# Kernel optimization log

Hardware: AMD Instinct MI355X
Metric: run time of the kernel (lower is better)

The kernel has to match this reference:

```python
import jax, jax.numpy as jnp
import numpy as np

DIST_THR = 0.2
CONTACT_TGT = 0.1
ALPHA = 0.01
HUBER_DELTA = 0.01
W_BCE = 0.5
W_DIST = 1.0
EPS = 1e-06


def setup_inputs() -> dict:
    key = jax.random.key(0)
    k1, k2, k3, k4 = jax.random.split(key, 4)
    BT, Vh, Vo = 16, 6890, 2048
    return {
        "human_verts": jax.random.uniform(k1, (BT, Vh, 3), dtype=jnp.float32),
        "object_verts": jax.random.uniform(k2, (BT, Vo, 3), dtype=jnp.float32),
        "gt_human_verts": jax.random.uniform(k3, (BT, Vh, 3), dtype=jnp.float32),
        "gt_object_verts": jax.random.uniform(k4, (BT, Vo, 3), dtype=jnp.float32),
    }


def _min_cdist(A, B):
    # A:[BT,NA,3], B:[BT,NB,3] -> min Euclidean distance over B: [BT,NA]
    aa = jnp.sum(A * A, axis=-1)               # [BT,NA]
    bb = jnp.sum(B * B, axis=-1)               # [BT,NB]
    ab = jnp.einsum("bnd,bmd->bnm", A, B)      # [BT,NA,NB]
    d2 = aa[:, :, None] + bb[:, None, :] - 2.0 * ab
    d = jnp.sqrt(jnp.maximum(d2, 0.0))
    return jnp.min(d, axis=-1)


def _bce_balanced(p, target):
    p = jnp.clip(p, 1e-06, 1.0 - 1e-06)
    pos = jnp.sum(target)
    neg = target.size - pos
    pos_w = (neg + EPS) / (pos + EPS)
    w = jnp.where(target > 0.5, pos_w, 1.0)
    loss = -(target * jnp.log(p) + (1.0 - target) * jnp.log(1.0 - p))
    return jnp.mean(w * loss)


def _masked_huber(over, mask):
    m = (mask > 0.5).astype(over.dtype)
    ax = jnp.abs(over)
    hub = jnp.where(ax < HUBER_DELTA, 0.5 * ax * ax / HUBER_DELTA, ax - 0.5 * HUBER_DELTA)
    cnt = jnp.sum(m)
    s = jnp.sum(hub * m)
    return jnp.where(cnt > 0, s / jnp.maximum(cnt, 1.0), 0.0)


def reference(human_verts, object_verts, gt_human_verts, gt_object_verts):
    dmin_h = _min_cdist(human_verts, object_verts)      # [BT,Vh]
    dmin_o = _min_cdist(object_verts, human_verts)      # [BT,Vo]
    dmin_h_gt = _min_cdist(gt_human_verts, gt_object_verts)
    dmin_o_gt = _min_cdist(gt_object_verts, gt_human_verts)
    gt_mask_h = (dmin_h_gt < DIST_THR).astype(jnp.float32)
    gt_mask_o = (dmin_o_gt < DIST_THR).astype(jnp.float32)

    inv_alpha = 1.0 / max(ALPHA, 1e-08)
    p_h = jax.nn.sigmoid((DIST_THR - dmin_h) * inv_alpha)
    p_o = jax.nn.sigmoid((DIST_THR - dmin_o) * inv_alpha)
    L_bce = 0.5 * (_bce_balanced(p_h, gt_mask_h) + _bce_balanced(p_o, gt_mask_o))

    over_h = jnp.maximum(dmin_h - CONTACT_TGT, 0.0)
    over_o = jnp.maximum(dmin_o - CONTACT_TGT, 0.0)
    L_dist = _masked_huber(over_h, gt_mask_h) + _masked_huber(over_o, gt_mask_o)

    return W_BCE * L_bce + W_DIST * L_dist
```

## Files before the change

### kernel.cpp

```cpp
#include <hip/hip_runtime.h>
#include <math.h>


#define BT 16
#define VH 6890
#define VO 2048
#define NH (BT * VH)
#define NO (BT * VO)

typedef float v2f __attribute__((ext_vector_type(2)));

#define RP 4

__global__ __launch_bounds__(256, 4)
void mindist_all(const float* __restrict__ hv,  const float* __restrict__ ov,
                 const float* __restrict__ ghv, const float* __restrict__ gov,
                 unsigned int* __restrict__ dh,  unsigned int* __restrict__ dov,
                 unsigned int* __restrict__ dhg, unsigned int* __restrict__ dog)
{
    __shared__ float4 lds[256];

    const int idx = blockIdx.x;
    const float *A, *B;
    unsigned int* out;
    int nA, nB, bt, abk, sliceLen, b0;

    if (idx < 1024) {
        const int p = idx >> 9;
        const int r = idx & 511;
        abk = r & 3;
        bt  = (r >> 2) & 15;
        const int z = r >> 6;
        A = p ? ghv : hv;  B = p ? gov : ov;  out = p ? dhg : dh;
        nA = VH; nB = VO; sliceLen = 256; b0 = z * 256;
    } else {
        const int q = idx - 1024;
        const int p = q >> 9;
        const int r = q & 511;
        abk = 0;
        bt  = r & 15;
        const int z = r >> 4;
        A = p ? gov : ov;  B = p ? ghv : hv;  out = p ? dog : dov;
        nA = VO; nB = VH; sliceLen = 216; b0 = z * 216;
    }

    const float* Ab = A + (size_t)bt * nA * 3;
    const float* Bb = B + (size_t)bt * nB * 3;
    const int tid = threadIdx.x;

    if (tid < sliceLen) {
        const int gj = b0 + tid;
        float4 w;
        if (gj < nB) {
            const float bx = Bb[gj * 3 + 0];
            const float by = Bb[gj * 3 + 1];
            const float bz = Bb[gj * 3 + 2];
            w = make_float4(-2.f * bx, -2.f * by, -2.f * bz,
                            fmaf(bx, bx, fmaf(by, by, bz * bz)));
        } else {
            w = make_float4(0.f, 0.f, 0.f, 3.0e38f);
        }
        lds[tid] = w;
    }

    const int rowb = abk * 2048 + tid;
    v2f ax[RP], ay[RP], az[RP], rmin[RP];
#pragma unroll
    for (int k = 0; k < RP; ++k) {
        const int r0 = rowb + (2 * k    ) * 256;
        const int r1 = rowb + (2 * k + 1) * 256;
        const int i0 = (r0 < nA) ? r0 : 0;
        const int i1 = (r1 < nA) ? r1 : 0;
        ax[k] = (v2f){Ab[i0 * 3 + 0], Ab[i1 * 3 + 0]};
        ay[k] = (v2f){Ab[i0 * 3 + 1], Ab[i1 * 3 + 1]};
        az[k] = (v2f){Ab[i0 * 3 + 2], Ab[i1 * 3 + 2]};
        rmin[k] = (v2f){3.0e38f, 3.0e38f};
    }

    __syncthreads();

    for (int j = 0; j < sliceLen; j += 4) {
#pragma unroll
        for (int u = 0; u < 4; ++u) {
            const float4 b = lds[j + u];
            const v2f nbx = (v2f){b.x, b.x};
            const v2f nby = (v2f){b.y, b.y};
            const v2f nbz = (v2f){b.z, b.z};
            const v2f bbv = (v2f){b.w, b.w};
#pragma unroll
            for (int k = 0; k < RP; ++k) {
                v2f t = __builtin_elementwise_fma(az[k], nbz, bbv);
                t     = __builtin_elementwise_fma(ay[k], nby, t);
                t     = __builtin_elementwise_fma(ax[k], nbx, t);
                rmin[k] = __builtin_elementwise_min(rmin[k], t);
            }
        }
    }

#pragma unroll
    for (int k = 0; k < RP; ++k) {
        const int r0 = rowb + (2 * k    ) * 256;
        const int r1 = rowb + (2 * k + 1) * 256;
        if (r0 < nA) {
            const float aa = fmaf(ax[k].x, ax[k].x, fmaf(ay[k].x, ay[k].x, az[k].x * az[k].x));
            const float v  = fmaxf(aa + rmin[k].x, 0.f);
            atomicMin(&out[(size_t)bt * nA + r0], __float_as_uint(v));
        }
        if (r1 < nA) {
            const float aa = fmaf(ax[k].y, ax[k].y, fmaf(ay[k].y, ay[k].y, az[k].y * az[k].y));
            const float v  = fmaxf(aa + rmin[k].y, 0.f);
            atomicMin(&out[(size_t)bt * nA + r1], __float_as_uint(v));
        }
    }
}

#define NBLK_H 431
#define NBLK_O 128

__global__ __launch_bounds__(256)
void reduce_loss_all(const float* __restrict__ dh2, const float* __restrict__ dhg2,
                     const float* __restrict__ do2, const float* __restrict__ dog2,
                     float* __restrict__ acc)
{
    const int b = blockIdx.x;
    const float *p2, *g2;
    float* a4;
    int N, i0;
    if (b < NBLK_H) { p2 = dh2; g2 = dhg2; a4 = acc;     N = NH; i0 = b * 256; }
    else            { p2 = do2; g2 = dog2; a4 = acc + 4; N = NO; i0 = (b - NBLK_H) * 256; }

    const int i = i0 + threadIdx.x;
    float t = 0.f, sp = 0.f, sn = 0.f, sh = 0.f;
    if (i < N) {
        const float d  = sqrtf(p2[i]);
        const float dg = sqrtf(g2[i]);
        const float tt = (dg < 0.2f) ? 1.f : 0.f;

        const float z = (0.2f - d) * 100.0f;
        float p = 1.0f / (1.0f + expf(-z));
        p = fminf(fmaxf(p, 1e-6f), 1.0f - 1e-6f);
        const float bce = (tt > 0.5f) ? -logf(p) : -logf(1.0f - p);

        const float over = fmaxf(d - 0.1f, 0.0f);
        const float hub  = (over < 0.01f) ? (0.5f * over * over) / 0.01f
                                          : (over - 0.5f * 0.01f);
        t  = tt;
        sp = tt * bce;
        sn = (1.0f - tt) * bce;
        sh = tt * hub;
    }
    for (int off = 32; off > 0; off >>= 1) {
        t  += __shfl_down(t,  off);
        sp += __shfl_down(sp, off);
        sn += __shfl_down(sn, off);
        sh += __shfl_down(sh, off);
    }
    __shared__ float wsum[4][4];
    const int wid = threadIdx.x >> 6, lane = threadIdx.x & 63;
    if (lane == 0) {
        wsum[wid][0] = t; wsum[wid][1] = sp; wsum[wid][2] = sn; wsum[wid][3] = sh;
    }
    __syncthreads();
    if (threadIdx.x == 0) {
        float s0 = 0, s1 = 0, s2 = 0, s3 = 0;
        for (int w = 0; w < 4; ++w) {
            s0 += wsum[w][0]; s1 += wsum[w][1]; s2 += wsum[w][2]; s3 += wsum[w][3];
        }
        atomicAdd(&a4[0], s0);
        atomicAdd(&a4[1], s1);
        atomicAdd(&a4[2], s2);
        atomicAdd(&a4[3], s3);
    }
}

__global__ void finalize_kernel(const float* __restrict__ acc, float* __restrict__ out)
{
    const float Ph = acc[0], SpH = acc[1], SnH = acc[2], ShH = acc[3];
    const float Po = acc[4], SpO = acc[5], SnO = acc[6], ShO = acc[7];
    const float Nh = (float)NH;
    const float No = (float)NO;

    const float pwH = ((Nh - Ph) + 1e-6f) / (Ph + 1e-6f);
    const float pwO = ((No - Po) + 1e-6f) / (Po + 1e-6f);
    const float bceH = (pwH * SpH + SnH) / Nh;
    const float bceO = (pwO * SpO + SnO) / No;
    const float Lbce = 0.5f * (bceH + bceO);

    const float LdH = (Ph > 0.f) ? ShH / fmaxf(Ph, 1.f) : 0.f;
    const float LdO = (Po > 0.f) ? ShO / fmaxf(Po, 1.f) : 0.f;
    const float Ldist = LdH + LdO;

    out[0] = 0.5f * Lbce + 1.0f * Ldist;
}

extern "C" void kernel_launch(void* const* d_in, const int* in_sizes, int n_in,
                              void* d_out, int out_size, void* d_ws, size_t ws_size,
                              hipStream_t stream)
{
    const float* hv  = (const float*)d_in[0];
    const float* ov  = (const float*)d_in[1];
    const float* ghv = (const float*)d_in[2];
    const float* gov = (const float*)d_in[3];

    float* ws  = (float*)d_ws;
    float* dh  = ws;
    float* dov = dh  + NH;
    float* dhg = dov + NO;
    float* dog = dhg + NH;
    float* acc = dog + NO;

    hipMemsetAsync(ws, 0x7f, (size_t)(2 * (NH + NO)) * sizeof(float), stream);
    hipMemsetAsync(acc, 0, 8 * sizeof(float), stream);

    mindist_all<<<2048, 256, 0, stream>>>(hv, ov, ghv, gov,
                                          (unsigned int*)dh, (unsigned int*)dov,
                                          (unsigned int*)dhg, (unsigned int*)dog);

    reduce_loss_all<<<NBLK_H + NBLK_O, 256, 0, stream>>>(dh, dhg, dov, dog, acc);

    finalize_kernel<<<1, 1, 0, stream>>>(acc, (float*)d_out);
}
```

Measured before the change: 163.6 us.

## Use inline packed FMA with op_sel broadcasts and min3, fuse finalize into reduce

The inner distance loop now uses inline-asm v_pk_fma_f32 with op_sel to broadcast B coordinates straight from packed LDS pairs, removing the per-element broadcast moves. It also merges two candidate minima with v_min3_f32. Launch bounds rise to 8 waves per SIMD to raise occupancy. The accumulator memset and the finalize kernel are replaced by zeroing inside the first kernel and a last-block-done pattern in the reduce kernel, which drops one memset and one launch. Risks are register pressure under the tighter launch bound and correctness of the hand-written op_sel encodings.

```diff
diff --git a/kernel.cpp b/kernel.cpp
--- a/kernel.cpp
+++ b/kernel.cpp
@@ -12,13 +12,28 @@
 
 #define RP 4
 
-__global__ __launch_bounds__(256, 4)
+#define PK_FMA_ZB(t, a, q) \
+    asm("v_pk_fma_f32 %0, %1, %2, %2 op_sel:[0,0,1] op_sel_hi:[1,0,1]" \
+        : "=v"(t) : "v"(a), "v"(q))
+#define PK_FMA_YB(t, a, p) \
+    asm("v_pk_fma_f32 %0, %1, %2, %0 op_sel:[0,1,0] op_sel_hi:[1,1,1]" \
+        : "+v"(t) : "v"(a), "v"(p))
+#define PK_FMA_XB(t, a, p) \
+    asm("v_pk_fma_f32 %0, %1, %2, %0 op_sel:[0,0,0] op_sel_hi:[1,0,1]" \
+        : "+v"(t) : "v"(a), "v"(p))
+#define MIN3(r, x, y) \
+    asm("v_min3_f32 %0, %1, %2, %0" : "+v"(r) : "v"(x), "v"(y))
+
+__global__ __launch_bounds__(256, 8)
 void mindist_all(const float* __restrict__ hv,  const float* __restrict__ ov,
                  const float* __restrict__ ghv, const float* __restrict__ gov,
                  unsigned int* __restrict__ dh,  unsigned int* __restrict__ dov,
-                 unsigned int* __restrict__ dhg, unsigned int* __restrict__ dog)
+                 unsigned int* __restrict__ dhg, unsigned int* __restrict__ dog,
+                 unsigned int* __restrict__ accw)
 {
-    __shared__ float4 lds[256];
+    __shared__ v2f lds2[512];
+
+    if (blockIdx.x == 0 && threadIdx.x < 12) accw[threadIdx.x] = 0u;
 
     const int idx = blockIdx.x;
     const float *A, *B;
@@ -50,21 +65,21 @@
 
     if (tid < sliceLen) {
         const int gj = b0 + tid;
-        float4 w;
         if (gj < nB) {
             const float bx = Bb[gj * 3 + 0];
             const float by = Bb[gj * 3 + 1];
             const float bz = Bb[gj * 3 + 2];
-            w = make_float4(-2.f * bx, -2.f * by, -2.f * bz,
-                            fmaf(bx, bx, fmaf(by, by, bz * bz)));
+            lds2[2 * tid + 0] = (v2f){-2.f * bx, -2.f * by};
+            lds2[2 * tid + 1] = (v2f){-2.f * bz, fmaf(bx, bx, fmaf(by, by, bz * bz))};
         } else {
-            w = make_float4(0.f, 0.f, 0.f, 3.0e38f);
-        }
-        lds[tid] = w;
+            lds2[2 * tid + 0] = (v2f){0.f, 0.f};
+            lds2[2 * tid + 1] = (v2f){0.f, 3.0e38f};
+        }
     }
 
     const int rowb = abk * 2048 + tid;
-    v2f ax[RP], ay[RP], az[RP], rmin[RP];
+    v2f ax[RP], ay[RP], az[RP];
+    float rx[RP], ry[RP];
 #pragma unroll
     for (int k = 0; k < RP; ++k) {
         const int r0 = rowb + (2 * k    ) * 256;
@@ -74,25 +89,30 @@
         ax[k] = (v2f){Ab[i0 * 3 + 0], Ab[i1 * 3 + 0]};
         ay[k] = (v2f){Ab[i0 * 3 + 1], Ab[i1 * 3 + 1]};
         az[k] = (v2f){Ab[i0 * 3 + 2], Ab[i1 * 3 + 2]};
-        rmin[k] = (v2f){3.0e38f, 3.0e38f};
+        rx[k] = 3.0e38f; ry[k] = 3.0e38f;
     }
 
     __syncthreads();
 
-    for (int j = 0; j < sliceLen; j += 4) {
-#pragma unroll
-        for (int u = 0; u < 4; ++u) {
-            const float4 b = lds[j + u];
-            const v2f nbx = (v2f){b.x, b.x};
-            const v2f nby = (v2f){b.y, b.y};
-            const v2f nbz = (v2f){b.z, b.z};
-            const v2f bbv = (v2f){b.w, b.w};
+    for (int j0 = 0; j0 < sliceLen; j0 += 8) {
+        const v2f* base = &lds2[2 * j0];
+#pragma unroll
+        for (int jj = 0; jj < 4; ++jj) {
+            const v2f p0 = base[4 * jj + 0];
+            const v2f q0 = base[4 * jj + 1];
+            const v2f p1 = base[4 * jj + 2];
+            const v2f q1 = base[4 * jj + 3];
 #pragma unroll
             for (int k = 0; k < RP; ++k) {
-                v2f t = __builtin_elementwise_fma(az[k], nbz, bbv);
-                t     = __builtin_elementwise_fma(ay[k], nby, t);
-                t     = __builtin_elementwise_fma(ax[k], nbx, t);
-                rmin[k] = __builtin_elementwise_min(rmin[k], t);
+                v2f tA, tB;
+                PK_FMA_ZB(tA, az[k], q0);
+                PK_FMA_YB(tA, ay[k], p0);
+                PK_FMA_XB(tA, ax[k], p0);
+                PK_FMA_ZB(tB, az[k], q1);
+                PK_FMA_YB(tB, ay[k], p1);
+                PK_FMA_XB(tB, ax[k], p1);
+                MIN3(rx[k], tA.x, tB.x);
+                MIN3(ry[k], tA.y, tB.y);
             }
         }
     }
@@ -103,24 +123,23 @@
         const int r1 = rowb + (2 * k + 1) * 256;
         if (r0 < nA) {
             const float aa = fmaf(ax[k].x, ax[k].x, fmaf(ay[k].x, ay[k].x, az[k].x * az[k].x));
-            const float v  = fmaxf(aa + rmin[k].x, 0.f);
-            atomicMin(&out[(size_t)bt * nA + r0], __float_as_uint(v));
+            atomicMin(&out[(size_t)bt * nA + r0], __float_as_uint(fmaxf(aa + rx[k], 0.f)));
         }
         if (r1 < nA) {
             const float aa = fmaf(ax[k].y, ax[k].y, fmaf(ay[k].y, ay[k].y, az[k].y * az[k].y));
-            const float v  = fmaxf(aa + rmin[k].y, 0.f);
-            atomicMin(&out[(size_t)bt * nA + r1], __float_as_uint(v));
+            atomicMin(&out[(size_t)bt * nA + r1], __float_as_uint(fmaxf(aa + ry[k], 0.f)));
         }
     }
 }
 
 #define NBLK_H 431
 #define NBLK_O 128
+#define NBLK   (NBLK_H + NBLK_O)
 
 __global__ __launch_bounds__(256)
-void reduce_loss_all(const float* __restrict__ dh2, const float* __restrict__ dhg2,
+void reduce_finalize(const float* __restrict__ dh2, const float* __restrict__ dhg2,
                      const float* __restrict__ do2, const float* __restrict__ dog2,
-                     float* __restrict__ acc)
+                     float* __restrict__ acc, float* __restrict__ outp)
 {
     const int b = blockIdx.x;
     const float *p2, *g2;
@@ -170,27 +189,28 @@
         atomicAdd(&a4[1], s1);
         atomicAdd(&a4[2], s2);
         atomicAdd(&a4[3], s3);
-    }
-}
-
-__global__ void finalize_kernel(const float* __restrict__ acc, float* __restrict__ out)
-{
-    const float Ph = acc[0], SpH = acc[1], SnH = acc[2], ShH = acc[3];
-    const float Po = acc[4], SpO = acc[5], SnO = acc[6], ShO = acc[7];
-    const float Nh = (float)NH;
-    const float No = (float)NO;
-
-    const float pwH = ((Nh - Ph) + 1e-6f) / (Ph + 1e-6f);
-    const float pwO = ((No - Po) + 1e-6f) / (Po + 1e-6f);
-    const float bceH = (pwH * SpH + SnH) / Nh;
-    const float bceO = (pwO * SpO + SnO) / No;
-    const float Lbce = 0.5f * (bceH + bceO);
-
-    const float LdH = (Ph > 0.f) ? ShH / fmaxf(Ph, 1.f) : 0.f;
-    const float LdO = (Po > 0.f) ? ShO / fmaxf(Po, 1.f) : 0.f;
-    const float Ldist = LdH + LdO;
-
-    out[0] = 0.5f * Lbce + 1.0f * Ldist;
+
+        __threadfence();
+        const unsigned f = atomicAdd((unsigned int*)&acc[8], 1u);
+        if (f == NBLK - 1) {
+            float v[8];
+            for (int q = 0; q < 8; ++q) v[q] = atomicAdd(&acc[q], 0.0f);
+            const float Ph = v[0], SpH = v[1], SnH = v[2], ShH = v[3];
+            const float Po = v[4], SpO = v[5], SnO = v[6], ShO = v[7];
+            const float Nh = (float)NH, No = (float)NO;
+
+            const float pwH = ((Nh - Ph) + 1e-6f) / (Ph + 1e-6f);
+            const float pwO = ((No - Po) + 1e-6f) / (Po + 1e-6f);
+            const float bceH = (pwH * SpH + SnH) / Nh;
+            const float bceO = (pwO * SpO + SnO) / No;
+            const float Lbce = 0.5f * (bceH + bceO);
+
+            const float LdH = (Ph > 0.f) ? ShH / fmaxf(Ph, 1.f) : 0.f;
+            const float LdO = (Po > 0.f) ? ShO / fmaxf(Po, 1.f) : 0.f;
+
+            outp[0] = 0.5f * Lbce + (LdH + LdO);
+        }
+    }
 }
 
 extern "C" void kernel_launch(void* const* d_in, const int* in_sizes, int n_in,
@@ -210,13 +230,11 @@
     float* acc = dog + NO;
 
     hipMemsetAsync(ws, 0x7f, (size_t)(2 * (NH + NO)) * sizeof(float), stream);
-    hipMemsetAsync(acc, 0, 8 * sizeof(float), stream);
 
     mindist_all<<<2048, 256, 0, stream>>>(hv, ov, ghv, gov,
                                           (unsigned int*)dh, (unsigned int*)dov,
-                                          (unsigned int*)dhg, (unsigned int*)dog);
-
-    reduce_loss_all<<<NBLK_H + NBLK_O, 256, 0, stream>>>(dh, dhg, dov, dog, acc);
-
-    finalize_kernel<<<1, 1, 0, stream>>>(acc, (float*)d_out);
+                                          (unsigned int*)dhg, (unsigned int*)dog,
+                                          (unsigned int*)acc);
+
+    reduce_finalize<<<NBLK, 256, 0, stream>>>(dh, dhg, dov, dog, acc, (float*)d_out);
 }
```

Result: slower. 172.3 us (+5.3%).
